# Optimization experiments

Hardware: AMD Instinct MI355X
Metric: run time of the kernel (lower is better)

## Reference

```python
import jax, jax.numpy as jnp
import numpy as np

S, K, O = 8192, 1024, 4096  # seq_len, in_features, out_features


def setup_inputs() -> dict:
    key = jax.random.key(0)
    k1, k2, k3, k4, k5 = jax.random.split(key, 5)
    x = jax.random.randint(k1, (S, K), -128, 128, dtype=jnp.int8)
    weight_q = jax.random.randint(k2, (O, K), -128, 128, dtype=jnp.int8)
    scale_x = jax.random.uniform(k3, (), jnp.float32, 0.01, 0.1)
    scale_w = jax.random.uniform(k4, (), jnp.float32, 0.01, 0.1)
    scale_y = jax.random.uniform(k5, (S,), jnp.float32, 0.5, 2.0)  # per-row output scale
    return {"x": x, "weight_q": weight_q, "scale_x": scale_x,
            "scale_w": scale_w, "scale_y": scale_y}


def reference(x, weight_q, scale_x, scale_w, scale_y):
    # int8 GEMM with int32 accumulation: [S,K] @ [O,K]^T -> [S,O]
    acc = jnp.einsum('sk,ok->so', x.astype(jnp.int32), weight_q.astype(jnp.int32))
    # fused per-row requantization: scale_y[:seq_len] gives per-row scale
    requant_scale = (scale_x * scale_w / scale_y).astype(jnp.float32)  # [S]
    scaled = acc.astype(jnp.float32) * requant_scale[:, None]
    out_q = jnp.clip(jnp.round(scaled), -128.0, 127.0).astype(jnp.int8)
    return out_q, scale_y
```

## Files before the change

### kernel.cpp

```cpp
#include <hip/hip_runtime.h>


#define S_DIM 8192
#define K_DIM 1024
#define O_DIM 4096
#define BM 128
#define BN 128
#define BK 64
#define NITER (K_DIM / BK)
#define TILE_BYTES (BM * BK)

using i32x4 = __attribute__((ext_vector_type(4))) int;

__global__ void pack_kernel(const int* __restrict__ xi, const int* __restrict__ wi,
                            const float* __restrict__ sy,
                            uint4* __restrict__ ap, uint4* __restrict__ bp,
                            float* __restrict__ out_sy) {
  const int tid = blockIdx.x * blockDim.x + threadIdx.x;
  const int nA = S_DIM * K_DIM / 16;
  const int nB = O_DIM * K_DIM / 16;

  const int4* src = nullptr;
  uint4* dst = nullptr;
  int j = 0;
  if (tid < nA) {
    j = tid; src = (const int4*)xi; dst = ap;
  } else if (tid < nA + nB) {
    j = tid - nA; src = (const int4*)wi; dst = bp;
  }
  if (dst) {
    const int t = j >> 9, idx = j & 511;
    const int sub = idx >> 6, q = (idx >> 4) & 3, fr = idx & 15;
    const int band = t >> 4, kt = t & 15;
    const int row = band * 128 + sub * 16 + fr;
    const int4* s4 = src + row * 256 + kt * 16 + q * 4;
    int4 v0 = s4[0], v1 = s4[1], v2 = s4[2], v3 = s4[3];
    uint4 o;
    o.x = (v0.x & 0xff) | ((v0.y & 0xff) << 8) | ((v0.z & 0xff) << 16) | (((unsigned)v0.w & 0xff) << 24);
    o.y = (v1.x & 0xff) | ((v1.y & 0xff) << 8) | ((v1.z & 0xff) << 16) | (((unsigned)v1.w & 0xff) << 24);
    o.z = (v2.x & 0xff) | ((v2.y & 0xff) << 8) | ((v2.z & 0xff) << 16) | (((unsigned)v2.w & 0xff) << 24);
    o.w = (v3.x & 0xff) | ((v3.y & 0xff) << 8) | ((v3.z & 0xff) << 16) | (((unsigned)v3.w & 0xff) << 24);
    dst[j] = o;
  }
  if (tid < S_DIM) out_sy[tid] = sy[tid];
}

__global__ __launch_bounds__(256, 3) void gemm_i8_kernel(
    const signed char* __restrict__ Ap,
    const signed char* __restrict__ Bp,
    const float* __restrict__ sx, const float* __restrict__ sw,
    const float* __restrict__ sy, float* __restrict__ out) {
  const int tid = threadIdx.x;
  const int wave = tid >> 6;
  const int lane = tid & 63;
  const int wm = wave >> 1;
  const int wn = wave & 1;
  const int rowBase = blockIdx.x * BM;
  const int colBase = blockIdx.y * BN;

  const signed char* gA = Ap + (size_t)blockIdx.x * NITER * TILE_BYTES +
                          wm * 4096 + lane * 16;
  const signed char* gB = Bp + (size_t)blockIdx.y * NITER * TILE_BYTES +
                          wn * 4096 + lane * 16;

  i32x4 acc[4][4] = {};
  i32x4 af[2][4], bf[2][4];

#pragma unroll
  for (int mi = 0; mi < 4; ++mi) {
    af[0][mi] = *(const i32x4*)(gA + mi * 1024);
    bf[0][mi] = *(const i32x4*)(gB + mi * 1024);
  }

#pragma unroll 2
  for (int it = 0; it < NITER; ++it) {
    const int p = it & 1;
    if (it + 1 < NITER) {
      const size_t goff = (size_t)(it + 1) * TILE_BYTES;
#pragma unroll
      for (int mi = 0; mi < 4; ++mi) {
        af[p ^ 1][mi] = *(const i32x4*)(gA + goff + mi * 1024);
        bf[p ^ 1][mi] = *(const i32x4*)(gB + goff + mi * 1024);
      }
    }
#pragma unroll
    for (int mi = 0; mi < 4; ++mi)
#pragma unroll
      for (int ni = 0; ni < 4; ++ni)
        acc[mi][ni] = __builtin_amdgcn_mfma_i32_16x16x64_i8(
            af[p][mi], bf[p][ni], acc[mi][ni], 0, 0, 0);
  }

  const float sxw = sx[0] * sw[0];
  const int fr = lane & 15;
  const int quad = lane >> 4;
#pragma unroll
  for (int mi = 0; mi < 4; ++mi) {
#pragma unroll
    for (int r = 0; r < 4; ++r) {
      const int s = rowBase + wm * 64 + mi * 16 + quad * 4 + r;
      const float rs = sxw / sy[s];
      float* orow = out + (size_t)s * O_DIM + colBase + wn * 64 + fr;
#pragma unroll
      for (int ni = 0; ni < 4; ++ni) {
        float f = rintf((float)acc[mi][ni][r] * rs);
        f = fminf(127.0f, fmaxf(-128.0f, f));
        orow[ni * 16] = f;
      }
    }
  }
}

extern "C" void kernel_launch(void* const* d_in, const int* in_sizes, int n_in,
                              void* d_out, int out_size, void* d_ws, size_t ws_size,
                              hipStream_t stream) {
  const int* x = (const int*)d_in[0];
  const int* w = (const int*)d_in[1];
  const float* sx = (const float*)d_in[2];
  const float* sw = (const float*)d_in[3];
  const float* sy = (const float*)d_in[4];
  float* out = (float*)d_out;

  uint4* ap = (uint4*)d_ws;
  uint4* bp = ap + (size_t)S_DIM * K_DIM / 16;

  const int total = S_DIM * K_DIM / 16 + O_DIM * K_DIM / 16;
  pack_kernel<<<(total + 255) / 256, 256, 0, stream>>>(
      x, w, sy, ap, bp, out + (size_t)S_DIM * O_DIM);

  dim3 grid(S_DIM / BM, O_DIM / BN);
  gemm_i8_kernel<<<grid, 256, 0, stream>>>(
      (const signed char*)ap, (const signed char*)bp, sx, sw, sy, out);
}
```

Before: 204.5 us.

## Compute each 128x128 tile with a single wave holding an 8x8 MFMA register tile

Replaces the four-wave 256-thread block, where each wave computes a 64x64 sub-tile, with one 64-thread wave that computes the whole 128x128 output tile using an 8x8 grid of 16x16 MFMA accumulators. Each A and B fragment loaded from global memory now feeds eight MFMAs instead of four, halving the global load traffic per MFMA. In exchange the wave needs about 256 accumulator VGPRs plus 64 for double-buffered fragments, which limits occupancy to about one wave per SIMD and leaves little room to hide latency. The loop unroll pragma is also dropped.

Measured after the change: 228.8 us. 1.12x slower.

```diff
diff --git a/kernel.cpp b/kernel.cpp
--- a/kernel.cpp
+++ b/kernel.cpp
@@ -4,11 +4,9 @@
 #define S_DIM 8192
 #define K_DIM 1024
 #define O_DIM 4096
-#define BM 128
-#define BN 128
 #define BK 64
 #define NITER (K_DIM / BK)
-#define TILE_BYTES (BM * BK)
+#define TILE_BYTES (128 * BK)
 
 using i32x4 = __attribute__((ext_vector_type(4))) int;
 
@@ -45,48 +43,41 @@
   if (tid < S_DIM) out_sy[tid] = sy[tid];
 }
 
-__global__ __launch_bounds__(256, 3) void gemm_i8_kernel(
+__global__ __launch_bounds__(64, 1) void gemm_i8_kernel(
     const signed char* __restrict__ Ap,
     const signed char* __restrict__ Bp,
     const float* __restrict__ sx, const float* __restrict__ sw,
     const float* __restrict__ sy, float* __restrict__ out) {
-  const int tid = threadIdx.x;
-  const int wave = tid >> 6;
-  const int lane = tid & 63;
-  const int wm = wave >> 1;
-  const int wn = wave & 1;
-  const int rowBase = blockIdx.x * BM;
-  const int colBase = blockIdx.y * BN;
+  const int lane = threadIdx.x;
+  const int rowBase = blockIdx.x * 128;
+  const int colBase = blockIdx.y * 128;
 
-  const signed char* gA = Ap + (size_t)blockIdx.x * NITER * TILE_BYTES +
-                          wm * 4096 + lane * 16;
-  const signed char* gB = Bp + (size_t)blockIdx.y * NITER * TILE_BYTES +
-                          wn * 4096 + lane * 16;
+  const signed char* gA = Ap + (size_t)blockIdx.x * NITER * TILE_BYTES + lane * 16;
+  const signed char* gB = Bp + (size_t)blockIdx.y * NITER * TILE_BYTES + lane * 16;
 
-  i32x4 acc[4][4] = {};
-  i32x4 af[2][4], bf[2][4];
+  i32x4 acc[8][8] = {};
+  i32x4 af[2][8], bf[2][8];
 
 #pragma unroll
-  for (int mi = 0; mi < 4; ++mi) {
-    af[0][mi] = *(const i32x4*)(gA + mi * 1024);
-    bf[0][mi] = *(const i32x4*)(gB + mi * 1024);
+  for (int s = 0; s < 8; ++s) {
+    af[0][s] = *(const i32x4*)(gA + s * 1024);
+    bf[0][s] = *(const i32x4*)(gB + s * 1024);
   }
 
-#pragma unroll 2
   for (int it = 0; it < NITER; ++it) {
     const int p = it & 1;
     if (it + 1 < NITER) {
       const size_t goff = (size_t)(it + 1) * TILE_BYTES;
 #pragma unroll
-      for (int mi = 0; mi < 4; ++mi) {
-        af[p ^ 1][mi] = *(const i32x4*)(gA + goff + mi * 1024);
-        bf[p ^ 1][mi] = *(const i32x4*)(gB + goff + mi * 1024);
+      for (int s = 0; s < 8; ++s) {
+        af[p ^ 1][s] = *(const i32x4*)(gA + goff + s * 1024);
+        bf[p ^ 1][s] = *(const i32x4*)(gB + goff + s * 1024);
       }
     }
 #pragma unroll
-    for (int mi = 0; mi < 4; ++mi)
+    for (int mi = 0; mi < 8; ++mi)
 #pragma unroll
-      for (int ni = 0; ni < 4; ++ni)
+      for (int ni = 0; ni < 8; ++ni)
         acc[mi][ni] = __builtin_amdgcn_mfma_i32_16x16x64_i8(
             af[p][mi], bf[p][ni], acc[mi][ni], 0, 0, 0);
   }
@@ -95,14 +86,14 @@
   const int fr = lane & 15;
   const int quad = lane >> 4;
 #pragma unroll
-  for (int mi = 0; mi < 4; ++mi) {
+  for (int mi = 0; mi < 8; ++mi) {
 #pragma unroll
     for (int r = 0; r < 4; ++r) {
-      const int s = rowBase + wm * 64 + mi * 16 + quad * 4 + r;
+      const int s = rowBase + mi * 16 + quad * 4 + r;
       const float rs = sxw / sy[s];
-      float* orow = out + (size_t)s * O_DIM + colBase + wn * 64 + fr;
+      float* orow = out + (size_t)s * O_DIM + colBase + fr;
 #pragma unroll
-      for (int ni = 0; ni < 4; ++ni) {
+      for (int ni = 0; ni < 8; ++ni) {
         float f = rintf((float)acc[mi][ni][r] * rs);
         f = fminf(127.0f, fmaxf(-128.0f, f));
         orow[ni * 16] = f;
@@ -128,7 +119,7 @@
   pack_kernel<<<(total + 255) / 256, 256, 0, stream>>>(
       x, w, sy, ap, bp, out + (size_t)S_DIM * O_DIM);
 
-  dim3 grid(S_DIM / BM, O_DIM / BN);
-  gemm_i8_kernel<<<grid, 256, 0, stream>>>(
+  dim3 grid(S_DIM / 128, O_DIM / 128);
+  gemm_i8_kernel<<<grid, 64, 0, stream>>>(
       (const signed char*)ap, (const signed char*)bp, sx, sw, sy, out);
 }
```
